# Kernel optimization log

Hardware: AMD Instinct MI355X
Metric: run time of the kernel (lower is better)

Reference implementation:

```python
import jax, jax.numpy as jnp
import numpy as np

NUM_STATES = 10000
B, S = 64, 4096


def setup_inputs() -> dict:
    key = jax.random.key(0)
    k1, k2, k3, k4 = jax.random.split(key, 4)
    seqs = jax.random.randint(k1, (B, S), 0, NUM_STATES)
    # ragged lengths in [S//2, S]; length = number of valid timesteps per sequence
    lengths = jax.random.randint(k2, (B,), S // 2, S + 1)
    initial_probs = jax.random.uniform(k3, (NUM_STATES,), dtype=jnp.float32)
    initial_probs = initial_probs / initial_probs.sum()
    transition_probs = jax.random.uniform(k4, (NUM_STATES, NUM_STATES), dtype=jnp.float32)
    transition_probs = transition_probs / transition_probs.sum(axis=1, keepdims=True)
    return {
        "seqs": seqs,
        "lengths": lengths,
        "initial_probs": initial_probs,
        "transition_probs": transition_probs,
    }


def reference(seqs, lengths, initial_probs, transition_probs):
    # seqs: [B, S] int state ids (padded); lengths: [B] valid timesteps per seq.
    # Equivalent to the PackedSequence loop: per sequence,
    #   ll_b = log init[x_0] + sum_{t=1}^{len_b-1} log trans[x_{t-1}, x_t]
    # then return -logsumexp_b(ll_b)  (as in the original forward).
    ll0 = jnp.log(initial_probs[seqs[:, 0]])                       # [B]
    trans_ll = jnp.log(transition_probs[seqs[:, :-1], seqs[:, 1:]])  # [B, S-1]
    # transition at step t (target index t in 1..S-1) is valid iff t < length
    valid = jnp.arange(1, S)[None, :] < lengths[:, None]           # [B, S-1]
    ll = ll0 + jnp.sum(jnp.where(valid, trans_ll, 0.0), axis=1)    # [B]
    return -jax.nn.logsumexp(ll)
```

## Files before the change

kernel.cpp:

```cpp
#include <hip/hip_runtime.h>
#include <hip/hip_bf16.h>


#define B_SEQ 64
#define S_LEN 4096
#define NSTATES 10000
#define P_BLOCKS 16
#define BLOCK_T 256

__global__ __launch_bounds__(BLOCK_T) void markov_partials(
    const int* __restrict__ seqs,
    const int* __restrict__ lengths,
    const float* __restrict__ trans,
    float* __restrict__ ws) {
    const int b = blockIdx.y;
    const int p = blockIdx.x;
    const int tid = threadIdx.x;

    const int len = lengths[b];
    const int t = p * BLOCK_T + tid + 1;

    float v = 0.0f;
    if (t < len) {
        const int s0 = seqs[b * S_LEN + t - 1];
        const int s1 = seqs[b * S_LEN + t];
        const float pr = trans[(long long)s0 * NSTATES + s1];
        v = __logf(pr);
    }

    #pragma unroll
    for (int off = 32; off > 0; off >>= 1)
        v += __shfl_down(v, off, 64);

    __shared__ float wsum[BLOCK_T / 64];
    const int wave = tid >> 6;
    const int lane = tid & 63;
    if (lane == 0) wsum[wave] = v;
    __syncthreads();
    if (tid == 0) {
        float total = 0.0f;
        #pragma unroll
        for (int w = 0; w < BLOCK_T / 64; ++w) total += wsum[w];
        ws[b * P_BLOCKS + p] = total;
    }
}

__global__ __launch_bounds__(64) void markov_finalize(
    const int* __restrict__ seqs,
    const float* __restrict__ init,
    const float* __restrict__ ws,
    float* __restrict__ out) {
    const int b = threadIdx.x;

    float ll = __logf(init[seqs[b * S_LEN]]);
    #pragma unroll
    for (int p = 0; p < P_BLOCKS; ++p)
        ll += ws[b * P_BLOCKS + p];

    float m = ll;
    #pragma unroll
    for (int off = 32; off > 0; off >>= 1)
        m = fmaxf(m, __shfl_down(m, off, 64));
    m = __shfl(m, 0, 64);

    float e = __expf(ll - m);
    #pragma unroll
    for (int off = 32; off > 0; off >>= 1)
        e += __shfl_down(e, off, 64);

    if (b == 0)
        out[0] = -(m + __logf(e));
}

extern "C" void kernel_launch(void* const* d_in, const int* in_sizes, int n_in,
                              void* d_out, int out_size, void* d_ws, size_t ws_size,
                              hipStream_t stream) {
    const int* seqs      = (const int*)d_in[0];
    const int* lengths   = (const int*)d_in[1];
    const float* init    = (const float*)d_in[2];
    const float* trans   = (const float*)d_in[3];
    float* out           = (float*)d_out;
    float* ws            = (float*)d_ws;

    dim3 grid(P_BLOCKS, B_SEQ);
    markov_partials<<<grid, BLOCK_T, 0, stream>>>(seqs, lengths, trans, ws);
    markov_finalize<<<1, 64, 0, stream>>>(seqs, init, ws, out);
}
```

Before: 440.3 us.

## Fuse partial sums and logsumexp finalize via atomics and last-block detection

Merges the two kernels into one: each block atomically adds its partial log-likelihood into a per-sequence accumulator, and the last block to finish (detected via an atomic counter) computes the logsumexp. Each thread now handles two timesteps, halving the block count, and indexing uses 32-bit unsigned math. A memset zeroes the workspace before launch. This removes a kernel launch at the cost of atomics, a memset, and possibly less memory-level parallelism.

Result: slower. 460.8 us (+4.7%).

```diff
diff --git a/kernel.cpp b/kernel.cpp
--- a/kernel.cpp
+++ b/kernel.cpp
@@ -1,88 +1,95 @@
 #include <hip/hip_runtime.h>
-#include <hip/hip_bf16.h>
 
 
 #define B_SEQ 64
 #define S_LEN 4096
 #define NSTATES 10000
-#define P_BLOCKS 16
-#define BLOCK_T 256
+#define TPB 256
+#define TPT 2
+#define BLOCKS_PER_SEQ (S_LEN / (TPB * TPT))
+#define NBLOCKS (B_SEQ * BLOCKS_PER_SEQ)
 
-__global__ __launch_bounds__(BLOCK_T) void markov_partials(
+#define WS_ZERO_BYTES 512
+
+__global__ __launch_bounds__(TPB) void markov_fused(
     const int* __restrict__ seqs,
     const int* __restrict__ lengths,
+    const float* __restrict__ init,
     const float* __restrict__ trans,
-    float* __restrict__ ws) {
-    const int b = blockIdx.y;
-    const int p = blockIdx.x;
+    float* __restrict__ ws,
+    float* __restrict__ out) {
+    const int blk = blockIdx.x;
+    const int b   = blk >> 3;
+    const int p   = blk & 7;
     const int tid = threadIdx.x;
 
     const int len = lengths[b];
-    const int t = p * BLOCK_T + tid + 1;
+    const int* __restrict__ seqb = seqs + b * S_LEN;
 
     float v = 0.0f;
-    if (t < len) {
-        const int s0 = seqs[b * S_LEN + t - 1];
-        const int s1 = seqs[b * S_LEN + t];
-        const float pr = trans[(long long)s0 * NSTATES + s1];
-        v = __logf(pr);
+    #pragma unroll
+    for (int k = 0; k < TPT; ++k) {
+        const int t = p * (TPB * TPT) + k * TPB + tid + 1;
+        if (t < len) {
+            const unsigned s0 = (unsigned)seqb[t - 1];
+            const unsigned s1 = (unsigned)seqb[t];
+            v += __logf(trans[s0 * (unsigned)NSTATES + s1]);
+        }
     }
 
     #pragma unroll
     for (int off = 32; off > 0; off >>= 1)
         v += __shfl_down(v, off, 64);
 
-    __shared__ float wsum[BLOCK_T / 64];
+    __shared__ float wsum[TPB / 64];
+    __shared__ int last_flag;
     const int wave = tid >> 6;
     const int lane = tid & 63;
     if (lane == 0) wsum[wave] = v;
     __syncthreads();
+
     if (tid == 0) {
         float total = 0.0f;
         #pragma unroll
-        for (int w = 0; w < BLOCK_T / 64; ++w) total += wsum[w];
-        ws[b * P_BLOCKS + p] = total;
+        for (int w = 0; w < TPB / 64; ++w) total += wsum[w];
+        atomicAdd(&ws[b], total);
+        __threadfence();
+        int prev = atomicAdd((int*)&ws[B_SEQ], 1);
+        last_flag = (prev == NBLOCKS - 1);
     }
-}
+    __syncthreads();
+    if (!last_flag) return;
 
-__global__ __launch_bounds__(64) void markov_finalize(
-    const int* __restrict__ seqs,
-    const float* __restrict__ init,
-    const float* __restrict__ ws,
-    float* __restrict__ out) {
-    const int b = threadIdx.x;
+    if (tid < B_SEQ) {
+        const int bb = tid;
+        float ll = atomicAdd(&ws[bb], 0.0f);
+        ll += __logf(init[seqs[bb * S_LEN]]);
 
-    float ll = __logf(init[seqs[b * S_LEN]]);
-    #pragma unroll
-    for (int p = 0; p < P_BLOCKS; ++p)
-        ll += ws[b * P_BLOCKS + p];
+        float m = ll;
+        #pragma unroll
+        for (int off = 32; off > 0; off >>= 1)
+            m = fmaxf(m, __shfl_down(m, off, 64));
+        m = __shfl(m, 0, 64);
 
-    float m = ll;
-    #pragma unroll
-    for (int off = 32; off > 0; off >>= 1)
-        m = fmaxf(m, __shfl_down(m, off, 64));
-    m = __shfl(m, 0, 64);
+        float e = __expf(ll - m);
+        #pragma unroll
+        for (int off = 32; off > 0; off >>= 1)
+            e += __shfl_down(e, off, 64);
 
-    float e = __expf(ll - m);
-    #pragma unroll
-    for (int off = 32; off > 0; off >>= 1)
-        e += __shfl_down(e, off, 64);
-
-    if (b == 0)
-        out[0] = -(m + __logf(e));
+        if (bb == 0) out[0] = -(m + __logf(e));
+    }
 }
 
 extern "C" void kernel_launch(void* const* d_in, const int* in_sizes, int n_in,
                               void* d_out, int out_size, void* d_ws, size_t ws_size,
                               hipStream_t stream) {
-    const int* seqs      = (const int*)d_in[0];
-    const int* lengths   = (const int*)d_in[1];
-    const float* init    = (const float*)d_in[2];
-    const float* trans   = (const float*)d_in[3];
-    float* out           = (float*)d_out;
-    float* ws            = (float*)d_ws;
+    const int* seqs    = (const int*)d_in[0];
+    const int* lengths = (const int*)d_in[1];
+    const float* init  = (const float*)d_in[2];
+    const float* trans = (const float*)d_in[3];
+    float* out         = (float*)d_out;
+    float* ws          = (float*)d_ws;
 
-    dim3 grid(P_BLOCKS, B_SEQ);
-    markov_partials<<<grid, BLOCK_T, 0, stream>>>(seqs, lengths, trans, ws);
-    markov_finalize<<<1, 64, 0, stream>>>(seqs, init, ws, out);
+    hipMemsetAsync(d_ws, 0, WS_ZERO_BYTES, stream);
+    markov_fused<<<NBLOCKS, TPB, 0, stream>>>(seqs, lengths, init, trans, ws, out);
 }
```
